# Optimization experiments

Measured on AMD Instinct MI355X. Metric: run time of the kernel, lower is better.

The kernel has to match this reference:

```python
import jax, jax.numpy as jnp
import numpy as np

B, S, F_IN, F_OUT = 8, 128, 768, 768
NUM_REL = 41           # num_dependencies + 1
NUM_LAYER = 2
N_HEAD, HID = 8, 96    # hidden_dim = embed_dim // n_head
EMB = 768


def setup_inputs() -> dict:
    key = jax.random.key(0)
    ks = jax.random.split(key, 14)
    s = 1.0 / np.sqrt(F_IN)
    inp = {
        "x": jax.random.normal(ks[0], (B, S, F_IN), dtype=jnp.float32),
        "adj": jax.random.uniform(ks[1], (B, NUM_REL, S, S), dtype=jnp.float32),
        "q": jax.random.normal(ks[2], (B, EMB), dtype=jnp.float32),
        # R-GCN params (stacked over layers)
        "w_rgcn": jax.random.uniform(ks[3], (NUM_LAYER, NUM_REL, F_IN, F_OUT), minval=-s, maxval=s),
        "score_w": jax.random.uniform(ks[4], (NUM_LAYER, F_OUT), minval=-s, maxval=s),
        "score_b": jax.random.uniform(ks[5], (NUM_LAYER,), minval=-s, maxval=s),
        # Attention params (stored as [in, out] for x @ W)
        "wk": jax.random.uniform(ks[6], (EMB, N_HEAD * HID), minval=-s, maxval=s),
        "bk": jnp.zeros((N_HEAD * HID,), jnp.float32),
        "wq": jax.random.uniform(ks[7], (EMB, N_HEAD * HID), minval=-s, maxval=s),
        "bq": jnp.zeros((N_HEAD * HID,), jnp.float32),
        "wbil": jax.random.uniform(ks[8], (HID, HID), minval=-1.0 / np.sqrt(HID), maxval=1.0 / np.sqrt(HID)),
        "wproj": jax.random.uniform(ks[9], (N_HEAD * HID, EMB), minval=-s, maxval=s),
        "bproj": jnp.zeros((EMB,), jnp.float32),
    }
    return inp


def _rgcn_layer(h, adj, w, sw, sb):
    # h: [B,S,I]; adj: [B,R,S,S]; w: [R,I,O]
    hidden = jnp.einsum("bsi,rio->brso", h, w)            # per-relation transform
    denom = jnp.sum(adj, axis=3, keepdims=True)           # [B,R,S,1]
    intm = jnp.einsum("brsk,brko->brso", adj, hidden)     # relation-wise aggregation
    div = intm / jnp.where(denom == 0, jnp.ones_like(denom), denom)
    logits = jnp.einsum("brso,o->brs", div, sw) + sb      # score Linear(out->1)
    r_coeffs = jax.nn.softmax(logits, axis=1)             # softmax over relations
    out = jnp.einsum("brso,brs->bso", div, r_coeffs)
    return jax.nn.relu(out)


def _attention(k, q, wk, bk, wq, bq, wbil, wproj, bproj):
    # k: [B,S,E]; q: [B,E] -> [B,1,E]
    q3 = q[:, None, :]
    kx = (k @ wk + bk).reshape(B, S, N_HEAD, HID)
    qx = (q3 @ wq + bq).reshape(B, 1, N_HEAD, HID)
    qw = jnp.einsum("bqhd,de->bqhe", qx, wbil)            # bi_linear score
    score = jnp.einsum("bqhe,bkhe->bhqk", qw, kx)
    attn = jax.nn.softmax(score, axis=-1)
    o = jnp.einsum("bhqk,bkhd->bqhd", attn, kx).reshape(B, 1, N_HEAD * HID)
    return o @ wproj + bproj                              # [B,1,EMB]


def reference(x, adj, q, w_rgcn, score_w, score_b, wk, bk, wq, bq, wbil, wproj, bproj):
    h = x
    for l in range(NUM_LAYER):
        h = _rgcn_layer(h, adj, w_rgcn[l], score_w[l], score_b[l])
    return _attention(h, q, wk, bk, wq, bq, wbil, wproj, bproj)
```

## Files before the change

kernel.cpp:

```cpp
#include <hip/hip_runtime.h>
#include <stdint.h>

#define B_ 8
#define S_ 128
#define R_ 41
#define F_ 768
#define NH_ 8
#define HID_ 96
#define BS_ (B_*S_)
#define SM_SCALE 256.0f
#define NG_ 21
#define NWV_ (R_*12)

typedef _Float16 f16;
typedef _Float16 f16x8 __attribute__((ext_vector_type(8)));
typedef _Float16 f16x4 __attribute__((ext_vector_type(4)));
typedef _Float16 f16x2 __attribute__((ext_vector_type(2)));
typedef float f32x4 __attribute__((ext_vector_type(4)));
typedef float f32x2 __attribute__((ext_vector_type(2)));

#define GLD16(gp, lp) __builtin_amdgcn_global_load_lds((const __attribute__((address_space(1))) uint32_t*)(gp), (__attribute__((address_space(3))) uint32_t*)(lp), 16, 0, 0)

__device__ __forceinline__ float wredsum(float v){
  #pragma unroll
  for (int o=32;o;o>>=1) v += __shfl_down(v,o,64);
  return v;
}

__global__ __launch_bounds__(256) void kPrep(const float* __restrict__ w_rgcn, const float* __restrict__ score_w,
                                             const float* __restrict__ wk, const float* __restrict__ x,
                                             const float* __restrict__ qin, const float* __restrict__ wq,
                                             f16* __restrict__ wT0, f16* __restrict__ wT1,
                                             float* __restrict__ v0, float* __restrict__ v1,
                                             f16* __restrict__ wkT, f16* __restrict__ h16T,
                                             float* __restrict__ qxpart) {
  __shared__ float sbuf[64*68];
  int bid = blockIdx.x;
  int tid = threadIdx.x;
  if (bid < 2*NWV_) {
    int l = (bid >= NWV_);
    int sub = bid - l*NWV_;
    const float* w = w_rgcn + (size_t)l*R_*F_*F_;
    const float* sw = score_w + l*F_;
    f16* wT = l ? wT1 : wT0;
    float* v = l ? v1 : v0;
    int it = sub % 12, r = sub / 12;
    int ri = tid >> 2, c = tid & 3;
    const float* srow = w + ((size_t)r*F_ + (it*64 + ri))*F_ + c*16;
    float vacc = 0.f;
    f32x4 cur[4];
    #pragma unroll
    for (int j=0;j<4;j++) cur[j] = *(const f32x4*)(srow + j*4);
    for (int ot = 0; ot < 12; ++ot) {
      f32x4 nxt[4];
      if (ot < 11) {
        const float* nsrc = srow + (ot+1)*64;
        #pragma unroll
        for (int j=0;j<4;j++) nxt[j] = *(const f32x4*)(nsrc + j*4);
      }
      const float* swp = sw + ot*64 + c*16;
      #pragma unroll
      for (int j=0;j<4;j++){
        f32x4 s4 = *(const f32x4*)(swp + j*4);
        vacc += cur[j].x*s4.x + cur[j].y*s4.y + cur[j].z*s4.z + cur[j].w*s4.w;
      }
      __syncthreads();
      #pragma unroll
      for (int j=0;j<4;j++) *(f32x4*)&sbuf[ri*68 + c*16 + j*4] = cur[j];
      __syncthreads();
      int ro = tid >> 2;
      f16 outv[16];
      #pragma unroll
      for (int j=0;j<16;j++) outv[j] = (f16)sbuf[(c*16+j)*68 + ro];
      f16* dst = wT + ((size_t)r*F_ + (ot*64+ro))*F_ + it*64 + c*16;
      *(f16x8*)dst = *(f16x8*)&outv[0];
      *(f16x8*)(dst+8) = *(f16x8*)&outv[8];
      if (ot < 11) {
        #pragma unroll
        for (int j=0;j<4;j++) cur[j] = nxt[j];
      }
    }
    vacc += __shfl_down(vacc, 1, 64);
    vacc += __shfl_down(vacc, 2, 64);
    if (c == 0) v[(size_t)r*F_ + it*64 + ri] = vacc;
  } else if (bid < 2*NWV_ + 144) {
    int sub = bid - 2*NWV_;
    int ot = sub % 12; int it = sub / 12;
    int ri = tid >> 2, c = tid & 3;
    const float* src = wk + (size_t)(it*64 + ri)*F_ + ot*64 + c*16;
    #pragma unroll
    for (int j=0;j<4;j++){
      f32x4 v4 = *(const f32x4*)(src + j*4);
      *(f32x4*)&sbuf[ri*68 + c*16 + j*4] = v4;
    }
    __syncthreads();
    int ro = tid >> 2;
    f16 outv[16];
    #pragma unroll
    for (int j=0;j<16;j++) outv[j] = (f16)sbuf[(c*16+j)*68 + ro];
    f16* dst = wkT + (size_t)(ot*64+ro)*F_ + it*64 + c*16;
    *(f16x8*)dst = *(f16x8*)&outv[0];
    *(f16x8*)(dst+8) = *(f16x8*)&outv[8];
  } else if (bid < 2*NWV_ + 144 + 192) {
    int sub = bid - (2*NWV_ + 144);
    int st = sub & 1; int ft = (sub>>1) % 12; int b = sub / 24;
    f16* t = (f16*)sbuf;
    int sl = tid>>2, c = tid&3;
    const float* src = x + ((size_t)b*S_ + st*64 + sl)*F_ + ft*64 + c*16;
    f16 tmp[16];
    #pragma unroll
    for (int j=0;j<16;j++) tmp[j] = (f16)src[j];
    *(f16x8*)&t[sl*72 + c*16]     = *(f16x8*)&tmp[0];
    *(f16x8*)&t[sl*72 + c*16 + 8] = *(f16x8*)&tmp[8];
    __syncthreads();
    int fl = tid>>2;
    f16 outv[16];
    #pragma unroll
    for (int j=0;j<16;j++) outv[j] = t[(c*16+j)*72 + fl];
    f16* dst = h16T + ((size_t)b*F_ + ft*64 + fl)*S_ + st*64 + c*16;
    *(f16x8*)dst = *(f16x8*)&outv[0];
    *(f16x8*)(dst+8) = *(f16x8*)&outv[8];
  } else {
    int sub = bid - (2*NWV_ + 144 + 192);
    int b = sub / 24; int rem = sub % 24;
    int seg = rem >> 3, i8 = rem & 7;
    float* q_s = sbuf;
    if (tid < 96) q_s[tid] = qin[(size_t)b*F_ + i8*96 + tid];
    __syncthreads();
    int col = seg*256 + tid;
    const float* wp = wq + (size_t)(i8*96)*F_ + col;
    float a0=0.f,a1=0.f,a2=0.f,a3=0.f,a4=0.f,a5=0.f,a6=0.f,a7=0.f;
    for (int i=0;i<96;i+=8){
      a0 += q_s[i]  *wp[(size_t)(i)*F_];
      a1 += q_s[i+1]*wp[(size_t)(i+1)*F_];
      a2 += q_s[i+2]*wp[(size_t)(i+2)*F_];
      a3 += q_s[i+3]*wp[(size_t)(i+3)*F_];
      a4 += q_s[i+4]*wp[(size_t)(i+4)*F_];
      a5 += q_s[i+5]*wp[(size_t)(i+5)*F_];
      a6 += q_s[i+6]*wp[(size_t)(i+6)*F_];
      a7 += q_s[i+7]*wp[(size_t)(i+7)*F_];
    }
    qxpart[((size_t)i8*B_ + b)*F_ + col] = ((a0+a1)+(a2+a3))+((a4+a5)+(a6+a7));
  }
}

__global__ __launch_bounds__(256) void kUL(const float* __restrict__ h, const float* __restrict__ v,
                    const float* __restrict__ adj, const float* __restrict__ sb_all, int l,
                    float* __restrict__ dinv, float* __restrict__ lg) {
  int bid = blockIdx.x;
  int r = bid % R_, b = bid / R_;
  __shared__ float v_s[F_];
  __shared__ float u_s[S_];
  int tid = threadIdx.x;
  #pragma unroll
  for (int j=0;j<3;j++) v_s[tid + j*256] = v[(size_t)r*F_ + tid + j*256];
  __syncthreads();
  int wid = tid>>6, lane = tid&63;
  for (int kl=0; kl<32; ++kl){
    int k = wid*32 + kl;
    const float* hr = h + ((size_t)b*S_ + k)*F_ + lane*12;
    const float* vp = &v_s[lane*12];
    float acc=0.f;
    #pragma unroll
    for (int j=0;j<3;j++){
      f32x4 a = *(const f32x4*)(hr+j*4);
      f32x4 c4 = *(const f32x4*)(vp+j*4);
      acc += a.x*c4.x+a.y*c4.y+a.z*c4.z+a.w*c4.w;
    }
    acc = wredsum(acc);
    if (lane==0) u_s[k] = acc;
  }
  __syncthreads();
  int s = tid>>1, half = tid&1;
  const float* arow = adj + ((size_t)bid*S_ + s)*S_ + half*64;
  const float* up = &u_s[half*64];
  float ssum=0.f, sdot=0.f;
  #pragma unroll
  for (int j=0;j<16;j++){
    f32x4 a = *(const f32x4*)(arow + j*4);
    ssum += a.x+a.y+a.z+a.w;
    sdot += a.x*up[j*4] + a.y*up[j*4+1] + a.z*up[j*4+2] + a.w*up[j*4+3];
  }
  ssum += __shfl_xor(ssum,1,64);
  sdot += __shfl_xor(sdot,1,64);
  if (half==0){
    float dv = (ssum==0.0f)?1.0f:(1.0f/ssum);
    dinv[(size_t)bid*S_ + s] = dv;
    lg[(size_t)bid*S_ + s] = sdot*dv + sb_all[l];
  }
}

__global__ __launch_bounds__(64) void kSM16(const float* __restrict__ lg, const float* __restrict__ dinv,
                     const float* __restrict__ adj, f16* __restrict__ M) {
  int bid = blockIdx.x;
  int b = bid >> 7, s = bid & 127;
  int lane = threadIdx.x;
  __shared__ float coef[R_];
  float x = (lane < R_) ? lg[((size_t)b*R_ + lane)*S_ + s] : -1e30f;
  float m = x;
  #pragma unroll
  for (int o=32;o;o>>=1) m = fmaxf(m, __shfl_xor(m,o,64));
  float e = (lane < R_) ? expf(x - m) : 0.f;
  float sum = e;
  #pragma unroll
  for (int o=32;o;o>>=1) sum += __shfl_xor(sum,o,64);
  if (lane < R_) coef[lane] = e/sum * SM_SCALE * dinv[((size_t)b*R_ + lane)*S_ + s];
  __syncthreads();
  for (int r=0;r<R_;r++){
    float cc = coef[r];
    size_t base = (((size_t)(b*R_+r))*S_ + s)*S_ + lane*2;
    f32x2 a2 = *(const f32x2*)(adj + base);
    f16x2 o2; o2[0]=(f16)(a2.x*cc); o2[1]=(f16)(a2.y*cc);
    *(f16x2*)(M + base) = o2;
  }
}

__global__ __launch_bounds__(256) void kGgemm(const f16* __restrict__ M, const f16* __restrict__ hT, f16* __restrict__ G) {
  __shared__ f16 lds[2*16384];
  f16* lsA = lds;
  f16* lsB = lds + 16384;
  int bid = blockIdx.x;
  int nt = bid % 6; int r = (bid/6) % R_; int b = bid/(6*R_);
  int tid = threadIdx.x, wid = tid>>6, lane = tid&63;
  const f16* Ab = M + (size_t)(b*R_ + r)*(S_*S_);
  const f16* Bb = hT + ((size_t)b*F_ + nt*128)*S_;
  #pragma unroll
  for (int j=0;j<8;j++){
    int qd = wid*8 + j;
    GLD16(Ab + qd*512 + lane*8, lsA + qd*512);
    GLD16(Bb + qd*512 + lane*8, lsB + qd*512);
  }
  __syncthreads();
  f32x4 acc[4][4] = {};
  int wr = wid>>1, wc = wid&1;
  int lr = lane&15, kk0 = (lane>>4)*8;
  #pragma unroll
  for (int ks=0;ks<4;ks++){
    int kk = ks*32 + kk0;
    f16x8 av[4], bv[4];
    #pragma unroll
    for (int i=0;i<4;i++) av[i] = *(const f16x8*)&lsA[(wr*64+i*16+lr)*128 + kk];
    #pragma unroll
    for (int i=0;i<4;i++) bv[i] = *(const f16x8*)&lsB[(wc*64+i*16+lr)*128 + kk];
    #pragma unroll
    for (int mi=0;mi<4;mi++)
      #pragma unroll
      for (int ni=0;ni<4;ni++)
        acc[mi][ni] = __builtin_amdgcn_mfma_f32_16x16x32_f16(av[mi],bv[ni],acc[mi][ni],0,0,0);
  }
  __syncthreads();
  #pragma unroll
  for (int mi=0;mi<4;mi++)
    #pragma unroll
    for (int ni=0;ni<4;ni++){
      int row = wr*64 + mi*16 + (lane>>4)*4;
      int col = wc*64 + ni*16 + lr;
      #pragma unroll
      for (int i=0;i<4;i++)
        lds[(row+i)*136 + col] = (f16)acc[mi][ni][i];
    }
  __syncthreads();
  int row = tid>>1, seg = tid&1;
  f16* dst = G + ((size_t)(b*R_ + r)*S_ + row)*F_ + nt*128 + seg*64;
  const f16* sl = lds + row*136 + seg*64;
  #pragma unroll
  for (int j=0;j<8;j++) *(f16x8*)(dst + j*8) = *(const f16x8*)(sl + j*8);
}

__global__ __launch_bounds__(512,2) void kOutGemm(const f16* __restrict__ G, const f16* __restrict__ WT, float* __restrict__ Cp) {
  __shared__ f16 ls[2][2][256*64];
  int bid = blockIdx.x;
  int t12 = bid % 12, g = bid / 12;
  int nt = t12 % 3, mt = t12 / 3;
  int r0 = (g<20)? 2*g : 40;
  int nr = (g<20)? 2 : 1;
  int tid = threadIdx.x, wid = tid>>6, lane = tid&63;
  size_t abase[4], bbase[4];
  #pragma unroll
  for (int j=0;j<4;j++){
    int chunk = wid*4 + j;
    int arow = mt*256 + chunk*8 + (lane>>3);
    int b = arow >> 7, s = arow & 127;
    abase[j] = ((size_t)b*R_*S_ + s)*(size_t)F_ + (lane&7)*8;
    int orow = nt*256 + chunk*8 + (lane>>3);
    bbase[j] = (size_t)orow*F_ + (lane&7)*8;
  }
  f32x4 acc[8][4] = {};
  int wr = wid>>2, wc = wid&3;
  int lr = lane&15, kk0 = (lane>>4)*8;
  int nsteps = nr*12;
  auto STAGE = [&](int bf, int step){
    int r = r0 + step/12, it = step%12;
    const f16* Ar = G  + (size_t)r*S_*F_;
    const f16* Br = WT + (size_t)r*F_*F_;
    #pragma unroll
    for (int j=0;j<4;j++){
      int chunk = wid*4 + j;
      GLD16(Ar + abase[j] + it*64, &ls[bf][0][chunk*512]);
      GLD16(Br + bbase[j] + it*64, &ls[bf][1][chunk*512]);
    }
  };
  STAGE(0, 0);
  __syncthreads();
  int cur = 0;
  for (int step=0; step<nsteps; ++step){
    if (step+1 < nsteps) STAGE(cur^1, step+1);
    __builtin_amdgcn_s_setprio(1);
    #pragma unroll
    for (int ks=0;ks<2;ks++){
      int kk = ks*32 + kk0;
      f16x8 av[8], bv[4];
      #pragma unroll
      for (int i=0;i<8;i++) av[i] = *(const f16x8*)&ls[cur][0][(wr*128+i*16+lr)*64 + kk];
      #pragma unroll
      for (int i=0;i<4;i++) bv[i] = *(const f16x8*)&ls[cur][1][(wc*64+i*16+lr)*64 + kk];
      #pragma unroll
      for (int mi=0;mi<8;mi++)
        #pragma unroll
        for (int ni=0;ni<4;ni++)
          acc[mi][ni] = __builtin_amdgcn_mfma_f32_16x16x32_f16(av[mi],bv[ni],acc[mi][ni],0,0,0);
    }
    __builtin_amdgcn_s_setprio(0);
    __syncthreads();
    cur ^= 1;
  }
  #pragma unroll
  for (int mi=0;mi<8;mi++)
    #pragma unroll
    for (int ni=0;ni<4;ni++){
      int row = mt*256 + wr*128 + mi*16 + (lane>>4)*4;
      int col = nt*256 + wc*64 + ni*16 + lr;
      #pragma unroll
      for (int i=0;i<4;i++)
        Cp[((size_t)g*BS_ + row + i)*F_ + col] = acc[mi][ni][i];
    }
}

__global__ __launch_bounds__(256) void kReduceT(const float* __restrict__ Cp, float* __restrict__ h32,
                                                f16* __restrict__ h16o, f16* __restrict__ hT) {
  int bid = blockIdx.x;
  int st = bid & 1; int ft = (bid>>1) % 12; int b = bid / 24;
  __shared__ f16 t[64*72];
  int tid = threadIdx.x;
  int sl = tid>>2, c = tid&3;
  size_t base = ((size_t)(b*S_ + st*64 + sl))*F_ + ft*64 + c*16;
  const float inv = 1.0f/SM_SCALE;
  f16 tmp[16];
  #pragma unroll
  for (int q=0;q<4;q++){
    f32x4 s4 = {};
    #pragma unroll
    for (int g=0; g<NG_; g++){
      f32x4 v4 = *(const f32x4*)(Cp + (size_t)g*BS_*F_ + base + q*4);
      s4.x += v4.x; s4.y += v4.y; s4.z += v4.z; s4.w += v4.w;
    }
    f32x4 rr;
    rr.x = fmaxf(s4.x*inv, 0.f); rr.y = fmaxf(s4.y*inv, 0.f);
    rr.z = fmaxf(s4.z*inv, 0.f); rr.w = fmaxf(s4.w*inv, 0.f);
    *(f32x4*)(h32 + base + q*4) = rr;
    tmp[q*4+0]=(f16)rr.x; tmp[q*4+1]=(f16)rr.y; tmp[q*4+2]=(f16)rr.z; tmp[q*4+3]=(f16)rr.w;
  }
  *(f16x8*)&t[sl*72 + c*16]     = *(f16x8*)&tmp[0];
  *(f16x8*)&t[sl*72 + c*16 + 8] = *(f16x8*)&tmp[8];
  *(f16x8*)(h16o + base)     = *(f16x8*)&tmp[0];
  *(f16x8*)(h16o + base + 8) = *(f16x8*)&tmp[8];
  __syncthreads();
  int fl = tid>>2;
  f16 outv[16];
  #pragma unroll
  for (int j=0;j<16;j++) outv[j] = t[(c*16+j)*72 + fl];
  f16* dst = hT + ((size_t)b*F_ + ft*64 + fl)*S_ + st*64 + c*16;
  *(f16x8*)dst = *(f16x8*)&outv[0];
  *(f16x8*)(dst+8) = *(f16x8*)&outv[8];
}

__global__ __launch_bounds__(256) void kKx(const f16* __restrict__ A, const f16* __restrict__ BT,
                    const float* __restrict__ bias, float* __restrict__ C) {
  __shared__ f16 ls[2][2][128*64];
  int bid = blockIdx.x;
  int nt = bid % 6, mt = bid / 6;
  int tid = threadIdx.x, wid = tid>>6, lane = tid&63;
  size_t abase[4], bbase[4];
  #pragma unroll
  for (int j=0;j<4;j++){
    int qd = wid*4 + j;
    int row = mt*128 + qd*8 + (lane>>3);
    abase[j] = (size_t)row*F_ + (lane&7)*8;
    int o = nt*128 + qd*8 + (lane>>3);
    bbase[j] = (size_t)o*F_ + (lane&7)*8;
  }
  f32x4 acc[4][4] = {};
  int wr = wid>>1, wc = wid&1;
  int lr = lane&15, kk0 = (lane>>4)*8;
  auto STAGE = [&](int bf, int it){
    #pragma unroll
    for (int j=0;j<4;j++){
      int qd = wid*4+j;
      GLD16(A + abase[j] + it*64, &ls[bf][0][qd*512]);
      GLD16(BT + bbase[j] + it*64, &ls[bf][1][qd*512]);
    }
  };
  STAGE(0, 0);
  __syncthreads();
  int cur = 0;
  for (int it=0; it<12; ++it){
    if (it+1 < 12) STAGE(cur^1, it+1);
    #pragma unroll
    for (int ks=0;ks<2;ks++){
      int kk = ks*32 + kk0;
      f16x8 av[4], bv[4];
      #pragma unroll
      for (int i=0;i<4;i++) av[i] = *(const f16x8*)&ls[cur][0][(wr*64+i*16+lr)*64 + kk];
      #pragma unroll
      for (int i=0;i<4;i++) bv[i] = *(const f16x8*)&ls[cur][1][(wc*64+i*16+lr)*64 + kk];
      #pragma unroll
      for (int mi=0;mi<4;mi++)
        #pragma unroll
        for (int ni=0;ni<4;ni++)
          acc[mi][ni] = __builtin_amdgcn_mfma_f32_16x16x32_f16(av[mi],bv[ni],acc[mi][ni],0,0,0);
    }
    __syncthreads();
    cur ^= 1;
  }
  #pragma unroll
  for (int mi=0;mi<4;mi++)
    #pragma unroll
    for (int ni=0;ni<4;ni++){
      int row = mt*128 + wr*64 + mi*16 + (lane>>4)*4;
      int col = nt*128 + wc*64 + ni*16 + lr;
      float bb = bias[col];
      #pragma unroll
      for (int i=0;i<4;i++)
        C[(size_t)(row+i)*F_ + col] = acc[mi][ni][i] + bb;
    }
}

__global__ __launch_bounds__(256) void kAttnCore(const float* __restrict__ kx, const float* __restrict__ qxpart,
                                                 const float* __restrict__ bq, const float* __restrict__ wbil,
                                                 float* __restrict__ obuf) {
  int bid = blockIdx.x; int h = bid & 7; int b = bid >> 3;
  __shared__ float qx_s[HID_], qw_s[HID_], sc[S_];
  __shared__ float smax, ssum;
  int t = threadIdx.x;
  if (t < HID_) {
    float s = bq[h*HID_ + t];
    #pragma unroll
    for (int p=0;p<8;p++) s += qxpart[((size_t)p*B_ + b)*F_ + h*HID_ + t];
    qx_s[t] = s;
  }
  __syncthreads();
  if (t < HID_) {
    float a0=0.f,a1=0.f,a2=0.f,a3=0.f;
    for (int d=0;d<HID_;d+=4){
      a0 += qx_s[d]  *wbil[(size_t)d*HID_+t];
      a1 += qx_s[d+1]*wbil[(size_t)(d+1)*HID_+t];
      a2 += qx_s[d+2]*wbil[(size_t)(d+2)*HID_+t];
      a3 += qx_s[d+3]*wbil[(size_t)(d+3)*HID_+t];
    }
    qw_s[t] = a0+a1+a2+a3;
  }
  __syncthreads();
  {
    int k = t>>1, half = t&1;
    const float* kp = kx + ((size_t)b*S_ + k)*F_ + h*HID_ + half*48;
    const float* qp = &qw_s[half*48];
    float a0=0.f,a1=0.f;
    #pragma unroll
    for (int e=0;e<48;e+=8){
      f32x4 k0 = *(const f32x4*)(kp+e);
      f32x4 k1 = *(const f32x4*)(kp+e+4);
      a0 += k0.x*qp[e]+k0.y*qp[e+1]+k0.z*qp[e+2]+k0.w*qp[e+3];
      a1 += k1.x*qp[e+4]+k1.y*qp[e+5]+k1.z*qp[e+6]+k1.w*qp[e+7];
    }
    float s2 = a0+a1;
    s2 += __shfl_xor(s2,1,64);
    if (half==0) sc[k] = s2;
  }
  __syncthreads();
  if (t < 64) {
    float m = fmaxf(sc[t], sc[t+64]);
    #pragma unroll
    for (int o=32;o;o>>=1) m = fmaxf(m, __shfl_down(m,o,64));
    if (t==0) smax = m;
  }
  __syncthreads();
  if (t < S_) sc[t] = expf(sc[t]-smax);
  __syncthreads();
  if (t < 64) {
    float s = sc[t] + sc[t+64];
    s = wredsum(s);
    if (t==0) ssum = s;
  }
  __syncthreads();
  if (t < 192) {
    int d = t>>1, kh = (t&1)*64;
    const float* kp = kx + ((size_t)b*S_ + kh)*F_ + h*HID_ + d;
    float a0=0.f,a1=0.f,a2=0.f,a3=0.f;
    #pragma unroll
    for (int k=0;k<64;k+=4){
      a0 += sc[kh+k]  *kp[(size_t)k*F_];
      a1 += sc[kh+k+1]*kp[(size_t)(k+1)*F_];
      a2 += sc[kh+k+2]*kp[(size_t)(k+2)*F_];
      a3 += sc[kh+k+3]*kp[(size_t)(k+3)*F_];
    }
    float s2 = a0+a1+a2+a3;
    s2 += __shfl_xor(s2,1,64);
    if ((t&1)==0) obuf[(size_t)b*F_ + h*HID_ + d] = s2/ssum;
  }
}

__global__ __launch_bounds__(256) void kProj(const float* __restrict__ obuf, const float* __restrict__ wproj,
                      const float* __restrict__ bproj, float* __restrict__ outp) {
  int bid = blockIdx.x; int b = bid/3, seg = bid%3;
  int t = threadIdx.x;
  __shared__ float ov[F_];
  for (int j=t;j<F_;j+=256) ov[j] = obuf[(size_t)b*F_ + j];
  __syncthreads();
  int col = seg*256 + t;
  float a0=0.f,a1=0.f,a2=0.f,a3=0.f;
  for (int j=0;j<F_;j+=4){
    a0 += ov[j]*wproj[(size_t)j*F_+col];
    a1 += ov[j+1]*wproj[(size_t)(j+1)*F_+col];
    a2 += ov[j+2]*wproj[(size_t)(j+2)*F_+col];
    a3 += ov[j+3]*wproj[(size_t)(j+3)*F_+col];
  }
  outp[(size_t)b*F_ + col] = bproj[col] + a0+a1+a2+a3;
}

extern "C" void kernel_launch(void* const* d_in, const int* in_sizes, int n_in,
                              void* d_out, int out_size, void* d_ws, size_t ws_size,
                              hipStream_t stream) {
  (void)in_sizes; (void)n_in; (void)out_size;
  const float* x      = (const float*)d_in[0];
  const float* adj    = (const float*)d_in[1];
  const float* qin    = (const float*)d_in[2];
  const float* w_rgcn = (const float*)d_in[3];
  const float* score_w= (const float*)d_in[4];
  const float* score_b= (const float*)d_in[5];
  const float* wk     = (const float*)d_in[6];
  const float* bk     = (const float*)d_in[7];
  const float* wq     = (const float*)d_in[8];
  const float* bq     = (const float*)d_in[9];
  const float* wbil   = (const float*)d_in[10];
  const float* wproj  = (const float*)d_in[11];
  const float* bproj  = (const float*)d_in[12];
  float* outp = (float*)d_out;

  char* p = (char*)d_ws;
  auto alloc = [&](size_t bytes)->char* {
    char* r = p; p += (bytes + 255) & ~(size_t)255; return r;
  };
  f16*   w16T0 = (f16*)  alloc((size_t)R_*F_*F_*2);
  f16*   w16T1 = (f16*)  alloc((size_t)R_*F_*F_*2);
  f16*   G16   = (f16*)  alloc((size_t)B_*R_*S_*F_*2);
  f16*   M16   = (f16*)  alloc((size_t)B_*R_*S_*S_*2);
  float* Cpart = (float*)alloc((size_t)NG_*BS_*F_*4);
  float* h32a  = (float*)alloc((size_t)BS_*F_*4);
  f16*   h16row= (f16*)  alloc((size_t)BS_*F_*2);
  f16*   h16T  = (f16*)  alloc((size_t)BS_*F_*2);
  float* kx    = (float*)alloc((size_t)BS_*F_*4);
  f16*   wkT   = (f16*)  alloc((size_t)F_*F_*2);
  float* vbuf0 = (float*)alloc((size_t)R_*F_*4);
  float* vbuf1 = (float*)alloc((size_t)R_*F_*4);
  float* dinv  = (float*)alloc((size_t)B_*R_*S_*4);
  float* lgb   = (float*)alloc((size_t)B_*R_*S_*4);
  float* qxpart= (float*)alloc((size_t)8*B_*F_*4);
  float* obuf  = (float*)alloc((size_t)B_*F_*4);
  if ((size_t)(p - (char*)d_ws) > ws_size) return;

  kPrep<<<2*NWV_ + 144 + 192 + 192, 256, 0, stream>>>(
      w_rgcn, score_w, wk, x, qin, wq,
      w16T0, w16T1, vbuf0, vbuf1, wkT, h16T, qxpart);

  kUL<<<B_*R_, 256, 0, stream>>>(x, vbuf0, adj, score_b, 0, dinv, lgb);
  kSM16<<<B_*S_, 64, 0, stream>>>(lgb, dinv, adj, M16);
  kGgemm<<<B_*R_*6, 256, 0, stream>>>(M16, h16T, G16);
  kOutGemm<<<12*NG_, 512, 0, stream>>>(G16, w16T0, Cpart);
  kReduceT<<<192, 256, 0, stream>>>(Cpart, h32a, h16row, h16T);

  kUL<<<B_*R_, 256, 0, stream>>>(h32a, vbuf1, adj, score_b, 1, dinv, lgb);
  kSM16<<<B_*S_, 64, 0, stream>>>(lgb, dinv, adj, M16);
  kGgemm<<<B_*R_*6, 256, 0, stream>>>(M16, h16T, G16);
  kOutGemm<<<12*NG_, 512, 0, stream>>>(G16, w16T1, Cpart);
  kReduceT<<<192, 256, 0, stream>>>(Cpart, h32a, h16row, h16T);

  kKx<<<48, 256, 0, stream>>>(h16row, wkT, bk, kx);
  kAttnCore<<<64, 256, 0, stream>>>(kx, qxpart, bq, wbil, obuf);
  kProj<<<24, 256, 0, stream>>>(obuf, wproj, bproj, outp);
}
```

Baseline: 471.6 us.

## Convert adj to fp16 once and fold softmax row scaling into Ggemm epilogue

Removes the per-layer kSM16 kernel, which read the fp32 adjacency and wrote a scaled fp16 copy. Adjacency is now converted to fp16 once in the prep kernel and shared by both layers. The per-row softmax-over-relations coefficient is computed inside each Ggemm block and applied to the accumulator rows in the epilogue. Each of the 1968 Ggemm blocks now recomputes a 41-way softmax per row, reading all relations' logits, which adds redundant global reads and exp work. Rounding also changes because scaling now happens after the fp16 matmul rather than before.

Result: slower. 540.3 us (+14.6%).

```diff
diff --git a/kernel.cpp b/kernel.cpp
--- a/kernel.cpp
+++ b/kernel.cpp
@@ -11,6 +11,7 @@
 #define SM_SCALE 256.0f
 #define NG_ 21
 #define NWV_ (R_*12)
+#define NADJC_ 1312
 
 typedef _Float16 f16;
 typedef _Float16 f16x8 __attribute__((ext_vector_type(8)));
@@ -30,10 +31,11 @@
 __global__ __launch_bounds__(256) void kPrep(const float* __restrict__ w_rgcn, const float* __restrict__ score_w,
                                              const float* __restrict__ wk, const float* __restrict__ x,
                                              const float* __restrict__ qin, const float* __restrict__ wq,
+                                             const float* __restrict__ adj,
                                              f16* __restrict__ wT0, f16* __restrict__ wT1,
                                              float* __restrict__ v0, float* __restrict__ v1,
                                              f16* __restrict__ wkT, f16* __restrict__ h16T,
-                                             float* __restrict__ qxpart) {
+                                             float* __restrict__ qxpart, f16* __restrict__ adj16) {
   __shared__ float sbuf[64*68];
   int bid = blockIdx.x;
   int tid = threadIdx.x;
@@ -120,7 +122,7 @@
     f16* dst = h16T + ((size_t)b*F_ + ft*64 + fl)*S_ + st*64 + c*16;
     *(f16x8*)dst = *(f16x8*)&outv[0];
     *(f16x8*)(dst+8) = *(f16x8*)&outv[8];
-  } else {
+  } else if (bid < 2*NWV_ + 144 + 192 + 192) {
     int sub = bid - (2*NWV_ + 144 + 192);
     int b = sub / 24; int rem = sub % 24;
     int seg = rem >> 3, i8 = rem & 7;
@@ -141,6 +143,15 @@
       a7 += q_s[i+7]*wp[(size_t)(i+7)*F_];
     }
     qxpart[((size_t)i8*B_ + b)*F_ + col] = ((a0+a1)+(a2+a3))+((a4+a5)+(a6+a7));
+  } else {
+    int sub = bid - (2*NWV_ + 144 + 192 + 192);
+    size_t base = (size_t)sub*4096 + tid*4;
+    #pragma unroll
+    for (int j=0;j<4;j++){
+      f32x4 a4 = *(const f32x4*)(adj + base + j*1024);
+      f16x4 o4; o4[0]=(f16)a4.x; o4[1]=(f16)a4.y; o4[2]=(f16)a4.z; o4[3]=(f16)a4.w;
+      *(f16x4*)(adj16 + base + j*1024) = o4;
+    }
   }
 }
 
@@ -190,39 +201,17 @@
   }
 }
 
-__global__ __launch_bounds__(64) void kSM16(const float* __restrict__ lg, const float* __restrict__ dinv,
-                     const float* __restrict__ adj, f16* __restrict__ M) {
-  int bid = blockIdx.x;
-  int b = bid >> 7, s = bid & 127;
-  int lane = threadIdx.x;
-  __shared__ float coef[R_];
-  float x = (lane < R_) ? lg[((size_t)b*R_ + lane)*S_ + s] : -1e30f;
-  float m = x;
-  #pragma unroll
-  for (int o=32;o;o>>=1) m = fmaxf(m, __shfl_xor(m,o,64));
-  float e = (lane < R_) ? expf(x - m) : 0.f;
-  float sum = e;
-  #pragma unroll
-  for (int o=32;o;o>>=1) sum += __shfl_xor(sum,o,64);
-  if (lane < R_) coef[lane] = e/sum * SM_SCALE * dinv[((size_t)b*R_ + lane)*S_ + s];
-  __syncthreads();
-  for (int r=0;r<R_;r++){
-    float cc = coef[r];
-    size_t base = (((size_t)(b*R_+r))*S_ + s)*S_ + lane*2;
-    f32x2 a2 = *(const f32x2*)(adj + base);
-    f16x2 o2; o2[0]=(f16)(a2.x*cc); o2[1]=(f16)(a2.y*cc);
-    *(f16x2*)(M + base) = o2;
-  }
-}
-
-__global__ __launch_bounds__(256) void kGgemm(const f16* __restrict__ M, const f16* __restrict__ hT, f16* __restrict__ G) {
+__global__ __launch_bounds__(256) void kGgemm(const f16* __restrict__ A16, const f16* __restrict__ hT,
+                                              const float* __restrict__ lg, const float* __restrict__ dinv,
+                                              f16* __restrict__ G) {
   __shared__ f16 lds[2*16384];
+  __shared__ float coefS[S_];
   f16* lsA = lds;
   f16* lsB = lds + 16384;
   int bid = blockIdx.x;
   int nt = bid % 6; int r = (bid/6) % R_; int b = bid/(6*R_);
   int tid = threadIdx.x, wid = tid>>6, lane = tid&63;
-  const f16* Ab = M + (size_t)(b*R_ + r)*(S_*S_);
+  const f16* Ab = A16 + (size_t)(b*R_ + r)*(S_*S_);
   const f16* Bb = hT + ((size_t)b*F_ + nt*128)*S_;
   #pragma unroll
   for (int j=0;j<8;j++){
@@ -230,6 +219,15 @@
     GLD16(Ab + qd*512 + lane*8, lsA + qd*512);
     GLD16(Bb + qd*512 + lane*8, lsB + qd*512);
   }
+  if (tid < S_) {
+    int s = tid;
+    float m = -1e30f;
+    for (int rr=0; rr<R_; ++rr) m = fmaxf(m, lg[((size_t)(b*R_+rr))*S_ + s]);
+    float sum = 0.f;
+    for (int rr=0; rr<R_; ++rr) sum += expf(lg[((size_t)(b*R_+rr))*S_ + s] - m);
+    float e = expf(lg[((size_t)(b*R_+r))*S_ + s] - m);
+    coefS[s] = e/sum * SM_SCALE * dinv[((size_t)(b*R_+r))*S_ + s];
+  }
   __syncthreads();
   f32x4 acc[4][4] = {};
   int wr = wid>>1, wc = wid&1;
@@ -257,7 +255,7 @@
       int col = wc*64 + ni*16 + lr;
       #pragma unroll
       for (int i=0;i<4;i++)
-        lds[(row+i)*136 + col] = (f16)acc[mi][ni][i];
+        lds[(row+i)*136 + col] = (f16)(acc[mi][ni][i] * coefS[row+i]);
     }
   __syncthreads();
   int row = tid>>1, seg = tid&1;
@@ -553,7 +551,7 @@
   f16*   w16T0 = (f16*)  alloc((size_t)R_*F_*F_*2);
   f16*   w16T1 = (f16*)  alloc((size_t)R_*F_*F_*2);
   f16*   G16   = (f16*)  alloc((size_t)B_*R_*S_*F_*2);
-  f16*   M16   = (f16*)  alloc((size_t)B_*R_*S_*S_*2);
+  f16*   adj16 = (f16*)  alloc((size_t)B_*R_*S_*S_*2);
   float* Cpart = (float*)alloc((size_t)NG_*BS_*F_*4);
   float* h32a  = (float*)alloc((size_t)BS_*F_*4);
   f16*   h16row= (f16*)  alloc((size_t)BS_*F_*2);
@@ -568,19 +566,17 @@
   float* obuf  = (float*)alloc((size_t)B_*F_*4);
   if ((size_t)(p - (char*)d_ws) > ws_size) return;
 
-  kPrep<<<2*NWV_ + 144 + 192 + 192, 256, 0, stream>>>(
-      w_rgcn, score_w, wk, x, qin, wq,
-      w16T0, w16T1, vbuf0, vbuf1, wkT, h16T, qxpart);
+  kPrep<<<2*NWV_ + 144 + 192 + 192 + NADJC_, 256, 0, stream>>>(
+      w_rgcn, score_w, wk, x, qin, wq, adj,
+      w16T0, w16T1, vbuf0, vbuf1, wkT, h16T, qxpart, adj16);
 
   kUL<<<B_*R_, 256, 0, stream>>>(x, vbuf0, adj, score_b, 0, dinv, lgb);
-  kSM16<<<B_*S_, 64, 0, stream>>>(lgb, dinv, adj, M16);
-  kGgemm<<<B_*R_*6, 256, 0, stream>>>(M16, h16T, G16);
+  kGgemm<<<B_*R_*6, 256, 0, stream>>>(adj16, h16T, lgb, dinv, G16);
   kOutGemm<<<12*NG_, 512, 0, stream>>>(G16, w16T0, Cpart);
   kReduceT<<<192, 256, 0, stream>>>(Cpart, h32a, h16row, h16T);
 
   kUL<<<B_*R_, 256, 0, stream>>>(h32a, vbuf1, adj, score_b, 1, dinv, lgb);
-  kSM16<<<B_*S_, 64, 0, stream>>>(lgb, dinv, adj, M16);
-  kGgemm<<<B_*R_*6, 256, 0, stream>>>(M16, h16T, G16);
+  kGgemm<<<B_*R_*6, 256, 0, stream>>>(adj16, h16T, lgb, dinv, G16);
   kOutGemm<<<12*NG_, 512, 0, stream>>>(G16, w16T1, Cpart);
   kReduceT<<<192, 256, 0, stream>>>(Cpart, h32a, h16row, h16T);
 
```
